# Optimization experiments

Hardware: AMD Instinct MI355X
Metric: run time of the kernel (lower is better)

## Reference

```python
import jax, jax.numpy as jnp
import numpy as np

N = 65536   # batch
G = 7       # grid
C = 2       # classes (cats vs dogs)
A = 3       # anchors


def _bce(p, t):
    return -(t * jnp.log(p) + (1.0 - t) * jnp.log(1.0 - p))


def _iou(a, b):
    # a, b: [..., 4] boxes in (cx, cy, w, h) format
    ax1, ay1 = a[..., 0] - a[..., 2] / 2, a[..., 1] - a[..., 3] / 2
    ax2, ay2 = a[..., 0] + a[..., 2] / 2, a[..., 1] + a[..., 3] / 2
    bx1, by1 = b[..., 0] - b[..., 2] / 2, b[..., 1] - b[..., 3] / 2
    bx2, by2 = b[..., 0] + b[..., 2] / 2, b[..., 1] + b[..., 3] / 2
    iw = jnp.clip(jnp.minimum(ax2, bx2) - jnp.maximum(ax1, bx1), 0.0)
    ih = jnp.clip(jnp.minimum(ay2, by2) - jnp.maximum(ay1, by1), 0.0)
    inter = iw * ih
    union = (ax2 - ax1) * (ay2 - ay1) + (bx2 - bx1) * (by2 - by1) - inter
    return inter / (union + 1e-9)


def setup_inputs():
    key = jax.random.key(0)
    k1, k2, k3, k4 = jax.random.split(key, 4)
    # probabilities / box params must lie strictly in (0,1) for BCE and log()
    bbox_ = jax.random.uniform(k1, (N, 15, G, G), dtype=jnp.float32, minval=0.01, maxval=0.99)
    bbox = jax.random.uniform(k2, (N, 5, G, G), dtype=jnp.float32, minval=0.01, maxval=0.99)
    cls_ = jax.random.normal(k3, (N, C), dtype=jnp.float32)
    cls = jax.random.randint(k4, (N,), 1, 3).astype(jnp.int64)  # labels in {1,2}
    return {"bbox_": bbox_, "cls_": cls_, "bbox": bbox, "cls": cls}


def reference(bbox_, cls_, bbox, cls):
    n = bbox.shape[0]
    bidx = jnp.arange(n)

    # classification: CrossEntropyLoss (mean) with labels cls-1
    logp = jax.nn.log_softmax(cls_, axis=-1)
    ce = -jnp.mean(jnp.take_along_axis(logp, (cls - 1)[:, None], axis=1))

    # argmax cell of GT objectness map per sample
    probs = bbox[:, 0]                       # [N,7,7]
    m = jnp.argmax(probs.reshape(n, -1), axis=1)
    i, j = m // G, m % G                     # [N], [N]

    cell_gt = bbox[bidx, :, i, j]            # [N,5]
    cell_pr = bbox_[bidx, :, i, j].reshape(n, A, 5)  # [N,3,5]

    jf = j.astype(bbox.dtype)
    if_ = i.astype(bbox.dtype)

    # target box in global coords
    tgt = jnp.stack([(cell_gt[:, 1] + jf) / G, (cell_gt[:, 2] + if_) / G,
                     cell_gt[:, 3], cell_gt[:, 4]], axis=-1)          # [N,4]
    # anchor boxes in global coords
    anc = jnp.stack([(cell_pr[:, :, 1] + jf[:, None]) / G,
                     (cell_pr[:, :, 2] + if_[:, None]) / G,
                     cell_pr[:, :, 3], cell_pr[:, :, 4]], axis=-1)    # [N,3,4]

    best = jnp.argmax(_iou(anc, tgt[:, None, :]), axis=1)             # [N]

    # target objectness maps: best anchor channel gets GT prob map
    target_prob = jnp.zeros((n, A, G, G), dtype=bbox.dtype)
    target_prob = target_prob.at[bidx, best].set(probs)

    # coordinate BCE (sum) + size L1-of-logs (sum) at the matched cell/anchor
    best_box = cell_pr[bidx, best]           # [N,5]
    coord = jnp.sum(_bce(best_box[:, 1:3], cell_gt[:, 1:3]))
    size = jnp.sum(jnp.abs(jnp.log(best_box[:, 3:5]) - jnp.log(cell_gt[:, 3:5])))

    # per-anchor objectness BCE (mean over N*49 each)
    prob_loss = (jnp.mean(_bce(bbox_[:, 0], target_prob[:, 0]))
                 + jnp.mean(_bce(bbox_[:, 5], target_prob[:, 1]))
                 + jnp.mean(_bce(bbox_[:, 10], target_prob[:, 2])))

    return ce + coord + size + prob_loss
```

## Files before the change

kernel.cpp:

```cpp
#include <hip/hip_runtime.h>
#include <math.h>


static constexpr int GG  = 49;
static constexpr int PRD = 15 * GG;
static constexpr int GTD = 5  * GG;
static constexpr int SPG = 4;
static constexpr int PRC = SPG * PRD;
static constexpr int GTC = SPG * GTD;
static constexpr int PRB = PRC * 4;
static constexpr int GTB = GTC * 4;

__global__ void zero_kernel(float* out) { if (threadIdx.x == 0) out[0] = 0.0f; }

__device__ __forceinline__ void gload16(const float* g, float* l) {
    __builtin_amdgcn_global_load_lds(
        (const __attribute__((address_space(1))) void*)g,
        (__attribute__((address_space(3))) void*)l, 16, 0, 0);
}

__device__ __forceinline__ void stage_group(const float* __restrict__ prs,
                                            const float* __restrict__ gts,
                                            float* buf, int wslot, int lane) {
    #pragma unroll
    for (int u0 = 0; u0 < 3; ++u0) {
        const int u   = wslot + 4 * u0;
        const int rem = PRB - (u << 10);
        if ((lane << 4) < rem)
            gload16(prs + (u << 8) + (lane << 2), buf + (u << 8));
    }
    {   const int u   = wslot;
        const int rem = GTB - (u << 10);
        if ((lane << 4) < rem)
            gload16(gts + (u << 8) + (lane << 2), buf + PRC + (u << 8));
    }
}

__global__ __launch_bounds__(256) void loss_kernel(
    const float* __restrict__ pr_all,
    const float* __restrict__ cls_logits,
    const float* __restrict__ gt_all,
    const int*   __restrict__ cls_lbl,
    float* __restrict__ out, int N)
{
    const int lane  = threadIdx.x & 63;
    const int wslot = threadIdx.x >> 6;
    const float invG   = 1.0f / 7.0f;
    const float invN   = 1.0f / (float)N;
    const float invN49 = 1.0f / ((float)N * 49.0f);

    __shared__ float L[2][PRC + GTC];

    const int ngroups = N >> 2;
    const int per = (ngroups + gridDim.x - 1) / gridDim.x;
    const int gA  = blockIdx.x * per;
    const int gB  = min(gA + per, ngroups);

    float acc = 0.0f;
    int cur = 0;

    if (gA < gB)
        stage_group(pr_all + (size_t)gA * PRC, gt_all + (size_t)gA * GTC,
                    L[0], wslot, lane);
    __syncthreads();

    for (int g = gA; g < gB; ++g) {
        const int n = (g << 2) + wslot;

        const float x0 = cls_logits[2 * n];
        const float x1 = cls_logits[2 * n + 1];
        const int   cl = cls_lbl[n];

        if (g + 1 < gB)
            stage_group(pr_all + (size_t)(g + 1) * PRC,
                        gt_all + (size_t)(g + 1) * GTC,
                        L[cur ^ 1], wslot, lane);

        const float* Lp = L[cur];
        const float* Lg = L[cur] + PRC;
        const int pb_ = wslot * PRD;
        const int gb_ = wslot * GTD;

        const float t = (lane < GG) ? Lg[gb_ + lane] : -1.0f;
        float v = t;
        #pragma unroll
        for (int off = 32; off; off >>= 1) v = fmaxf(v, __shfl_xor(v, off));
        const unsigned long long eq = __ballot(t == v);
        const int m  = __ffsll(eq) - 1;
        const int mi = m / 7, mj = m - mi * 7;
        const float jf = (float)mj, if_ = (float)mi;

        const float g1v = Lg[gb_ +  49 + m];
        const float g2v = Lg[gb_ +  98 + m];
        const float g3v = Lg[gb_ + 147 + m];
        const float g4v = Lg[gb_ + 196 + m];

        const float tx  = (g1v + jf) * invG;
        const float ty  = (g2v + if_) * invG;
        const float tx1 = tx - g3v * 0.5f, tx2 = tx + g3v * 0.5f;
        const float ty1 = ty - g4v * 0.5f, ty2 = ty + g4v * 0.5f;
        const float tarea = (tx2 - tx1) * (ty2 - ty1);

        int best = 0; float bestIoU = -1.0f;
        float px = 0.f, py = 0.f, pw = 0.f, ph = 0.f;
        #pragma unroll
        for (int a = 0; a < 3; a++) {
            const float c1 = Lp[pb_ + (5 * a + 1) * GG + m];
            const float c2 = Lp[pb_ + (5 * a + 2) * GG + m];
            const float c3 = Lp[pb_ + (5 * a + 3) * GG + m];
            const float c4 = Lp[pb_ + (5 * a + 4) * GG + m];
            const float ax  = (c1 + jf) * invG;
            const float ay  = (c2 + if_) * invG;
            const float ax1 = ax - c3 * 0.5f, ax2 = ax + c3 * 0.5f;
            const float ay1 = ay - c4 * 0.5f, ay2 = ay + c4 * 0.5f;
            float iw = fminf(ax2, tx2) - fmaxf(ax1, tx1); iw = fmaxf(iw, 0.0f);
            float ih = fminf(ay2, ty2) - fmaxf(ay1, ty1); ih = fmaxf(ih, 0.0f);
            const float inter = iw * ih;
            const float uni   = (ax2 - ax1) * (ay2 - ay1) + tarea - inter;
            const float iou   = inter / (uni + 1e-9f);
            if (iou > bestIoU) { bestIoU = iou; best = a; px = c1; py = c2; pw = c3; ph = c4; }
        }

        float s = 0.0f;
        if (lane < GG) {
            const float p0 = Lp[pb_ +           lane];
            const float p1 = Lp[pb_ + 5 * GG  + lane];
            const float p2 = Lp[pb_ + 10 * GG + lane];
            const float l0 = __logf(1.0f - p0);
            const float l1 = __logf(1.0f - p1);
            const float l2 = __logf(1.0f - p2);
            s = -(l0 + l1 + l2);
            const float pbv  = (best == 0) ? p0 : (best == 1) ? p1 : p2;
            const float l1pb = (best == 0) ? l0 : (best == 1) ? l1 : l2;
            s -= t * (__logf(pbv) - l1pb);
        }
        acc += s * invN49;

        const float s0  = (lane < 4) ? ((lane < 2) ? px : py)
                                     : ((lane < 6) ? pw : ph);
        const float s1  = (lane < 4) ? (1.0f - s0)
                                     : ((lane < 6) ? g3v : g4v);
        const float la  = (lane & 1) ? s1 : s0;
        const float Lv  = __logf(la);
        const float Lx  = __shfl_xor(Lv, 1);
        float contrib = 0.0f;
        if (lane < 4) {
            const float w = (lane < 2) ? ((lane & 1) ? 1.0f - g1v : g1v)
                                       : ((lane & 1) ? 1.0f - g2v : g2v);
            contrib = -w * Lv;
        } else if (lane == 4 || lane == 6) {
            contrib = fabsf(Lv - Lx);
        }
        acc += contrib;

        if (lane == 5) {
            const float mx  = fmaxf(x0, x1);
            const float lse = mx + __logf(1.0f + __expf(-fabsf(x0 - x1)));
            const float lp  = ((cl == 1) ? x0 : x1) - lse;
            acc -= lp * invN;
        }

        __syncthreads();
        cur ^= 1;
    }

    #pragma unroll
    for (int off = 32; off; off >>= 1) acc += __shfl_xor(acc, off);
    __shared__ float wsum[4];
    if (lane == 0) wsum[wslot] = acc;
    __syncthreads();
    if (threadIdx.x == 0) {
        atomicAdd(out, wsum[0] + wsum[1] + wsum[2] + wsum[3]);
    }
}

extern "C" void kernel_launch(void* const* d_in, const int* in_sizes, int n_in,
                              void* d_out, int out_size, void* d_ws, size_t ws_size,
                              hipStream_t stream) {
    const float* bbox_p = (const float*)d_in[0];
    const float* cls_p  = (const float*)d_in[1];
    const float* bbox_g = (const float*)d_in[2];
    const int*   cls_l  = (const int*)d_in[3];
    float* out = (float*)d_out;
    const int N = in_sizes[3];

    hipLaunchKernelGGL(zero_kernel, dim3(1), dim3(64), 0, stream, out);
    hipLaunchKernelGGL(loss_kernel, dim3(2048), dim3(256), 0, stream,
                       bbox_p, cls_p, bbox_g, cls_l, out, N);
}
```

Measured before the change: 317.4 us.

## Replace block-level async LDS double buffering with per-wave register loads

Drops the block-wide double-buffered global_load_lds staging and the per-iteration __syncthreads. Each wave now handles one sample at a time in a grid-stride loop: it loads the sample's prediction and ground-truth data into registers with nontemporal loads, then writes them into its own private LDS slice for the gathered accesses. Removing block barriers lets waves run independently, at the cost of losing explicit prefetch overlap within a wave, so latency hiding now depends on occupancy.

```diff
diff --git a/kernel.cpp b/kernel.cpp
--- a/kernel.cpp
+++ b/kernel.cpp
@@ -5,36 +5,10 @@
 static constexpr int GG  = 49;
 static constexpr int PRD = 15 * GG;
 static constexpr int GTD = 5  * GG;
-static constexpr int SPG = 4;
-static constexpr int PRC = SPG * PRD;
-static constexpr int GTC = SPG * GTD;
-static constexpr int PRB = PRC * 4;
-static constexpr int GTB = GTC * 4;
+static constexpr int GOF = 768;
+static constexpr int LPW = 1024;
 
 __global__ void zero_kernel(float* out) { if (threadIdx.x == 0) out[0] = 0.0f; }
-
-__device__ __forceinline__ void gload16(const float* g, float* l) {
-    __builtin_amdgcn_global_load_lds(
-        (const __attribute__((address_space(1))) void*)g,
-        (__attribute__((address_space(3))) void*)l, 16, 0, 0);
-}
-
-__device__ __forceinline__ void stage_group(const float* __restrict__ prs,
-                                            const float* __restrict__ gts,
-                                            float* buf, int wslot, int lane) {
-    #pragma unroll
-    for (int u0 = 0; u0 < 3; ++u0) {
-        const int u   = wslot + 4 * u0;
-        const int rem = PRB - (u << 10);
-        if ((lane << 4) < rem)
-            gload16(prs + (u << 8) + (lane << 2), buf + (u << 8));
-    }
-    {   const int u   = wslot;
-        const int rem = GTB - (u << 10);
-        if ((lane << 4) < rem)
-            gload16(gts + (u << 8) + (lane << 2), buf + PRC + (u << 8));
-    }
-}
 
 __global__ __launch_bounds__(256) void loss_kernel(
     const float* __restrict__ pr_all,
@@ -45,43 +19,55 @@
 {
     const int lane  = threadIdx.x & 63;
     const int wslot = threadIdx.x >> 6;
+    const int wid   = blockIdx.x * (blockDim.x >> 6) + wslot;
+    const int nwaves = gridDim.x * (blockDim.x >> 6);
     const float invG   = 1.0f / 7.0f;
     const float invN   = 1.0f / (float)N;
     const float invN49 = 1.0f / ((float)N * 49.0f);
 
-    __shared__ float L[2][PRC + GTC];
-
-    const int ngroups = N >> 2;
-    const int per = (ngroups + gridDim.x - 1) / gridDim.x;
-    const int gA  = blockIdx.x * per;
-    const int gB  = min(gA + per, ngroups);
+    __shared__ float L[4][LPW];
+    float* __restrict__ Lw = L[wslot];
 
     float acc = 0.0f;
-    int cur = 0;
 
-    if (gA < gB)
-        stage_group(pr_all + (size_t)gA * PRC, gt_all + (size_t)gA * GTC,
-                    L[0], wslot, lane);
-    __syncthreads();
+    for (int n = wid; n < N; n += nwaves) {
+        const float* pr = pr_all + (size_t)n * PRD;
+        const float* gt = gt_all + (size_t)n * GTD;
 
-    for (int g = gA; g < gB; ++g) {
-        const int n = (g << 2) + wslot;
+        const float x0 = __builtin_nontemporal_load(cls_logits + 2 * n);
+        const float x1 = __builtin_nontemporal_load(cls_logits + 2 * n + 1);
+        const int   cl = __builtin_nontemporal_load(cls_lbl + n);
 
-        const float x0 = cls_logits[2 * n];
-        const float x1 = cls_logits[2 * n + 1];
-        const int   cl = cls_lbl[n];
+        float p[12];
+        #pragma unroll
+        for (int k = 0; k < 12; ++k) {
+            int d = lane + 64 * k;
+            if (d > PRD - 1) d = PRD - 1;
+            p[k] = __builtin_nontemporal_load(pr + d);
+        }
+        float g[4];
+        #pragma unroll
+        for (int k = 0; k < 4; ++k) {
+            int d = lane + 64 * k;
+            if (d > GTD - 1) d = GTD - 1;
+            g[k] = __builtin_nontemporal_load(gt + d);
+        }
 
-        if (g + 1 < gB)
-            stage_group(pr_all + (size_t)(g + 1) * PRC,
-                        gt_all + (size_t)(g + 1) * GTC,
-                        L[cur ^ 1], wslot, lane);
+        #pragma unroll
+        for (int k = 0; k < 12; ++k) {
+            int d = lane + 64 * k;
+            if (d > PRD - 1) d = PRD - 1;
+            Lw[d] = p[k];
+        }
+        #pragma unroll
+        for (int k = 0; k < 4; ++k) {
+            int d = lane + 64 * k;
+            if (d > GTD - 1) d = GTD - 1;
+            Lw[GOF + d] = g[k];
+        }
+        asm volatile("s_waitcnt lgkmcnt(0)" ::: "memory");
 
-        const float* Lp = L[cur];
-        const float* Lg = L[cur] + PRC;
-        const int pb_ = wslot * PRD;
-        const int gb_ = wslot * GTD;
-
-        const float t = (lane < GG) ? Lg[gb_ + lane] : -1.0f;
+        const float t = (lane < GG) ? g[0] : -1.0f;
         float v = t;
         #pragma unroll
         for (int off = 32; off; off >>= 1) v = fmaxf(v, __shfl_xor(v, off));
@@ -90,10 +76,10 @@
         const int mi = m / 7, mj = m - mi * 7;
         const float jf = (float)mj, if_ = (float)mi;
 
-        const float g1v = Lg[gb_ +  49 + m];
-        const float g2v = Lg[gb_ +  98 + m];
-        const float g3v = Lg[gb_ + 147 + m];
-        const float g4v = Lg[gb_ + 196 + m];
+        const float g1v = Lw[GOF +  49 + m];
+        const float g2v = Lw[GOF +  98 + m];
+        const float g3v = Lw[GOF + 147 + m];
+        const float g4v = Lw[GOF + 196 + m];
 
         const float tx  = (g1v + jf) * invG;
         const float ty  = (g2v + if_) * invG;
@@ -105,10 +91,10 @@
         float px = 0.f, py = 0.f, pw = 0.f, ph = 0.f;
         #pragma unroll
         for (int a = 0; a < 3; a++) {
-            const float c1 = Lp[pb_ + (5 * a + 1) * GG + m];
-            const float c2 = Lp[pb_ + (5 * a + 2) * GG + m];
-            const float c3 = Lp[pb_ + (5 * a + 3) * GG + m];
-            const float c4 = Lp[pb_ + (5 * a + 4) * GG + m];
+            const float c1 = Lw[(5 * a + 1) * GG + m];
+            const float c2 = Lw[(5 * a + 2) * GG + m];
+            const float c3 = Lw[(5 * a + 3) * GG + m];
+            const float c4 = Lw[(5 * a + 4) * GG + m];
             const float ax  = (c1 + jf) * invG;
             const float ay  = (c2 + if_) * invG;
             const float ax1 = ax - c3 * 0.5f, ax2 = ax + c3 * 0.5f;
@@ -123,9 +109,9 @@
 
         float s = 0.0f;
         if (lane < GG) {
-            const float p0 = Lp[pb_ +           lane];
-            const float p1 = Lp[pb_ + 5 * GG  + lane];
-            const float p2 = Lp[pb_ + 10 * GG + lane];
+            const float p0 = p[0];
+            const float p1 = Lw[5 * GG  + lane];
+            const float p2 = Lw[10 * GG + lane];
             const float l0 = __logf(1.0f - p0);
             const float l1 = __logf(1.0f - p1);
             const float l2 = __logf(1.0f - p2);
@@ -159,9 +145,6 @@
             const float lp  = ((cl == 1) ? x0 : x1) - lse;
             acc -= lp * invN;
         }
-
-        __syncthreads();
-        cur ^= 1;
     }
 
     #pragma unroll
```

Result: faster. 296.7 us (-6.5%).
